# Kernel optimization log

Measured on AMD Instinct MI355X. Metric: run time of the kernel, lower is better.

Reference implementation:

```python
import jax, jax.numpy as jnp
import numpy as np

NUM_EMBEDDINGS = 1024
EMBEDDING_DIM = 256


def setup_inputs() -> dict:
    key = jax.random.key(0)
    k1, k2 = jax.random.split(key)
    z = jax.random.normal(k1, (32, EMBEDDING_DIM, 32, 32), dtype=jnp.float32)
    codebook = jax.random.normal(k2, (NUM_EMBEDDINGS, EMBEDDING_DIM), dtype=jnp.float32)
    return {"z": z, "codebook": codebook}


def reference(z, codebook):
    # z: (B, C, H, W) -> (B, H, W, C) -> (B*H*W, C)
    B, C, H, W = z.shape
    z_bhwc = jnp.transpose(z, (0, 2, 3, 1))
    z_flat = z_bhwc.reshape(-1, C)  # (N, C)

    # pairwise squared distances: ||z||^2 + ||e||^2 - 2 z.e^T  -> (N, K)
    distances = (
        jnp.sum(z_flat ** 2, axis=1, keepdims=True)
        + jnp.sum(codebook ** 2, axis=1)
        - 2.0 * jnp.matmul(z_flat, codebook.T)
    )
    argmin_codewords = jnp.argmin(distances, axis=1)  # (N,)
    min_codewords = jax.nn.one_hot(argmin_codewords, NUM_EMBEDDINGS, dtype=jnp.float32)  # (N, K)

    # quantized latents via one-hot @ codebook, back to (B, C, H, W)
    z_quantized = jnp.matmul(min_codewords, codebook).reshape(B, H, W, C)
    z_quantized = jnp.transpose(z_quantized, (0, 3, 1, 2))
    return (min_codewords, z_quantized)
```

## Files before the change

kernel.cpp:

```cpp
#include <hip/hip_runtime.h>

#define N_ROWS 32768
#define K_CODES 1024
#define CDIM 256

typedef _Float16 half8 __attribute__((ext_vector_type(8)));
typedef _Float16 half4 __attribute__((ext_vector_type(4)));
typedef float floatx16 __attribute__((ext_vector_type(16)));
typedef unsigned long long ull;

#define WS_ZH   0ull
#define WS_ZL   16777216ull
#define WS_CBH  33554432ull
#define WS_CBL  34078720ull
#define WS_CBN  34603008ull
#define WS_PART 34607104ull
#define WS_IDX  36704256ull
#define WS_NEED 36835328ull

__device__ __forceinline__ void g2lds16(const void* g, void* l) {
    __builtin_amdgcn_global_load_lds(
        (const __attribute__((address_space(1))) void*)g,
        (__attribute__((address_space(3))) void*)l, 16, 0, 0);
}


__global__ __launch_bounds__(64) void cb_prep(const float* __restrict__ cb,
                                              _Float16* __restrict__ cbh,
                                              _Float16* __restrict__ cbl,
                                              float* __restrict__ cbn) {
    int k = blockIdx.x;
    int lane = threadIdx.x;
    float4 v = reinterpret_cast<const float4*>(cb + k * CDIM)[lane];
    float s0 = v.x * 32.f, s1 = v.y * 32.f, s2 = v.z * 32.f, s3 = v.w * 32.f;
    half4 hv, lv;
    hv[0] = (_Float16)s0; lv[0] = (_Float16)(s0 - (float)hv[0]);
    hv[1] = (_Float16)s1; lv[1] = (_Float16)(s1 - (float)hv[1]);
    hv[2] = (_Float16)s2; lv[2] = (_Float16)(s2 - (float)hv[2]);
    hv[3] = (_Float16)s3; lv[3] = (_Float16)(s3 - (float)hv[3]);
    size_t off = (size_t)((lane >> 3) * K_CODES + k) * 32 + ((lane * 4) & 31);
    *reinterpret_cast<half4*>(&cbh[off]) = hv;
    *reinterpret_cast<half4*>(&cbl[off]) = lv;
    float s = s0 * s0 + s1 * s1 + s2 * s2 + s3 * s3;
    #pragma unroll
    for (int off2 = 32; off2 > 0; off2 >>= 1) s += __shfl_down(s, off2);
    if (lane == 0) cbn[k] = s;
}

__global__ __launch_bounds__(256) void z_prep(const float* __restrict__ z,
                                              _Float16* __restrict__ zh,
                                              _Float16* __restrict__ zl) {
    __shared__ float t[64][68];
    int hwt = blockIdx.x & 15;
    int ct  = (blockIdx.x >> 4) & 3;
    int bb  = blockIdx.x >> 6;
    int tid = threadIdx.x;
    #pragma unroll
    for (int p = 0; p < 4; p++) {
        int e = p * 256 + tid;
        int c = e >> 4, h4 = e & 15;
        float4 v = *reinterpret_cast<const float4*>(
            &z[((bb * 256 + ct * 64 + c) << 10) + hwt * 64 + h4 * 4]);
        *reinterpret_cast<float4*>(&t[c][h4 * 4]) = v;
    }
    __syncthreads();
    #pragma unroll
    for (int p = 0; p < 4; p++) {
        int e = p * 256 + tid;
        int hw = e >> 4, c4 = e & 15;
        half4 hv, lv;
        #pragma unroll
        for (int j = 0; j < 4; j++) {
            float s = t[c4 * 4 + j][hw] * 32.f;
            _Float16 h = (_Float16)s;
            hv[j] = h;
            lv[j] = (_Float16)(s - (float)h);
        }
        int n = bb * 1024 + hwt * 64 + hw;
        int cg = ct * 64 + c4 * 4;
        size_t off = (size_t)((cg >> 5) * N_ROWS + n) * 32 + (cg & 31);
        *reinterpret_cast<half4*>(&zh[off]) = hv;
        *reinterpret_cast<half4*>(&zl[off]) = lv;
    }
}

__global__ __launch_bounds__(256, 2) void vq_mfma32(
    const _Float16* __restrict__ zh, const _Float16* __restrict__ zl,
    const _Float16* __restrict__ cbh, const _Float16* __restrict__ cbl,
    const float* __restrict__ cbn, ull* __restrict__ partial) {

    __shared__ _Float16 AhL[8192], AlL[8192];
    __shared__ _Float16 BhL[4096], BlL[4096];
    __shared__ float rvv[256][2];
    __shared__ int   rcc[256][2];

    const int tid = threadIdx.x;
    const int lane = tid & 63, wave = tid >> 6;
    const int wm = wave & 1, wn = wave >> 1;
    const int fm = lane & 31, fq = lane >> 5;
    const int codeTile = blockIdx.x & 7;
    const int rowTile  = blockIdx.x >> 3;
    const int rowBase = rowTile * 256, codeBase = codeTile * 128;

    floatx16 acc[8];
    #pragma unroll
    for (int i = 0; i < 8; i++) acc[i] = (floatx16)0.f;

    for (int kc = 0; kc < CDIM; kc += 32) {
        const int cc = kc >> 5;
        const size_t ab = (size_t)(cc * N_ROWS + rowBase) * 32;
        const size_t bb = (size_t)(cc * K_CODES + codeBase) * 32;
        #pragma unroll
        for (int i = 0; i < 4; i++) {
            int G = i * 256 + tid;
            int q = G >> 8, r = G & 255;
            size_t so = (size_t)r * 32 + q * 8;
            g2lds16(zh + ab + so, &AhL[G * 8]);
            g2lds16(zl + ab + so, &AlL[G * 8]);
        }
        #pragma unroll
        for (int i = 0; i < 2; i++) {
            int G = i * 256 + tid;
            int q = G >> 7, r = G & 127;
            size_t so = (size_t)r * 32 + q * 8;
            g2lds16(cbh + bb + so, &BhL[G * 8]);
            g2lds16(cbl + bb + so, &BlL[G * 8]);
        }
        __syncthreads();
        #pragma unroll
        for (int s = 0; s < 2; s++) {
            int q = s * 2 + fq;
            half8 ah[4], al[4], bh[2], bl[2];
            #pragma unroll
            for (int i = 0; i < 4; i++) {
                int ga = q * 256 + wm * 128 + i * 32 + fm;
                ah[i] = *reinterpret_cast<const half8*>(&AhL[ga * 8]);
                al[i] = *reinterpret_cast<const half8*>(&AlL[ga * 8]);
            }
            #pragma unroll
            for (int j = 0; j < 2; j++) {
                int gb = q * 128 + wn * 64 + j * 32 + fm;
                bh[j] = *reinterpret_cast<const half8*>(&BhL[gb * 8]);
                bl[j] = *reinterpret_cast<const half8*>(&BlL[gb * 8]);
            }
            #pragma unroll
            for (int i = 0; i < 4; i++)
                #pragma unroll
                for (int j = 0; j < 2; j++) {
                    acc[i*2+j] = __builtin_amdgcn_mfma_f32_32x32x16_f16(ah[i], bh[j], acc[i*2+j], 0, 0, 0);
                    acc[i*2+j] = __builtin_amdgcn_mfma_f32_32x32x16_f16(al[i], bh[j], acc[i*2+j], 0, 0, 0);
                    acc[i*2+j] = __builtin_amdgcn_mfma_f32_32x32x16_f16(ah[i], bl[j], acc[i*2+j], 0, 0, 0);
                }
        }
        __syncthreads();
    }

    float cbnv[2];
    #pragma unroll
    for (int j = 0; j < 2; j++) cbnv[j] = cbn[codeBase + wn * 64 + j * 32 + fm];

    #pragma unroll
    for (int i = 0; i < 4; i++)
        #pragma unroll
        for (int r = 0; r < 16; r++) {
            float best = 3.4e38f; int bcode = 0x7fffffff;
            #pragma unroll
            for (int j = 0; j < 2; j++) {
                float d = fmaf(-2.f, acc[i*2+j][r], cbnv[j]);
                int code = codeBase + wn * 64 + j * 32 + fm;
                if (d < best) { best = d; bcode = code; }
            }
            #pragma unroll
            for (int m = 1; m < 32; m <<= 1) {
                float ov = __shfl_xor(best, m, 64);
                int   oc = __shfl_xor(bcode, m, 64);
                if (ov < best || (ov == best && oc < bcode)) { best = ov; bcode = oc; }
            }
            if (fm == 0) {
                int row = wm * 128 + i * 32 + (r & 3) + 8 * (r >> 2) + 4 * fq;
                rvv[row][wn] = best;
                rcc[row][wn] = bcode;
            }
        }
    __syncthreads();
    {
        float v0 = rvv[tid][0]; int c0 = rcc[tid][0];
        float v1 = rvv[tid][1]; int c1 = rcc[tid][1];
        if (v1 < v0 || (v1 == v0 && c1 < c0)) { v0 = v1; c0 = c1; }
        unsigned u = __float_as_uint(v0);
        u = (u & 0x80000000u) ? ~u : (u | 0x80000000u);
        partial[(size_t)(rowBase + tid) * 8 + codeTile] =
            ((ull)u << 32) | (unsigned)c0;
    }
}

__global__ __launch_bounds__(256) void onehot_fin(const ull* __restrict__ partial,
                                                  int* __restrict__ idx,
                                                  float* __restrict__ out) {
    int row = blockIdx.x;
    __shared__ int sid;
    if (threadIdx.x < 64) {
        ull v = (threadIdx.x < 8) ? partial[(size_t)row * 8 + threadIdx.x]
                                  : ~0ull;
        #pragma unroll
        for (int m = 1; m < 8; m <<= 1) {
            ull o = __shfl_xor(v, m, 64);
            if (o < v) v = o;
        }
        if (threadIdx.x == 0) {
            int id = (int)(v & 0xffffffffu);
            sid = id;
            idx[row] = id;
        }
    }
    __syncthreads();
    int id = sid;
    int k4 = threadIdx.x << 2;
    float4 v4;
    v4.x = (k4     == id) ? 1.f : 0.f;
    v4.y = (k4 + 1 == id) ? 1.f : 0.f;
    v4.z = (k4 + 2 == id) ? 1.f : 0.f;
    v4.w = (k4 + 3 == id) ? 1.f : 0.f;
    reinterpret_cast<float4*>(out)[(size_t)row * 256 + threadIdx.x] = v4;
}

__global__ __launch_bounds__(256) void zq_fill(const int* __restrict__ idx,
                                               const float* __restrict__ cb,
                                               float* __restrict__ out) {
    int i  = blockIdx.x * 256 + threadIdx.x;
    int hw = i & 1023;
    int c  = (i >> 10) & 255;
    int b  = i >> 18;
    int n  = (b << 10) | hw;
    out[i] = cb[idx[n] * CDIM + c];
}


__global__ __launch_bounds__(64) void cb_norms(const float* __restrict__ cb,
                                               float* __restrict__ cbn) {
    int k = blockIdx.x;
    int lane = threadIdx.x;
    float4 v = reinterpret_cast<const float4*>(cb + k * CDIM)[lane];
    float s = v.x * v.x + v.y * v.y + v.z * v.z + v.w * v.w;
    #pragma unroll
    for (int off = 32; off > 0; off >>= 1) s += __shfl_down(s, off);
    if (lane == 0) cbn[k] = s;
}

__global__ __launch_bounds__(256) void cb_transpose(const float* __restrict__ cb,
                                                    float* __restrict__ cbt) {
    __shared__ float t[32][33];
    int k0 = (blockIdx.x & 31) * 32;
    int c0 = (blockIdx.x >> 5) * 32;
    int lane = threadIdx.x & 31;
    int row = threadIdx.x >> 5;
    #pragma unroll
    for (int s = 0; s < 4; s++) {
        int r = row + s * 8;
        t[r][lane] = cb[(k0 + r) * CDIM + c0 + lane];
    }
    __syncthreads();
    #pragma unroll
    for (int s = 0; s < 4; s++) {
        int r = row + s * 8;
        cbt[(c0 + r) * K_CODES + k0 + lane] = t[lane][r];
    }
}

__global__ __launch_bounds__(512, 2) void vq_argmin(const float* __restrict__ z,
                                                    const float* __restrict__ cbt,
                                                    const float* __restrict__ cbn,
                                                    int* __restrict__ idx_out) {
    __shared__ float As[64][128];
    __shared__ float Bs[64][256];

    const int tid = threadIdx.x;
    const int tx = tid & 31;
    const int ty = tid >> 5;
    const int rowBase = blockIdx.x * 128;
    const int bb = rowBase >> 10;
    const int hwBase = rowBase & 1023;

    float minv[8];
    int   mini[8];
    #pragma unroll
    for (int i = 0; i < 8; i++) { minv[i] = 3.4e38f; mini[i] = 0; }

    for (int kt = 0; kt < K_CODES; kt += 256) {
        float acc[2][2][4][4];
        #pragma unroll
        for (int a = 0; a < 2; a++)
            #pragma unroll
            for (int b = 0; b < 2; b++)
                #pragma unroll
                for (int i = 0; i < 4; i++)
                    #pragma unroll
                    for (int j = 0; j < 4; j++) acc[a][b][i][j] = 0.f;

        for (int ccb = 0; ccb < CDIM; ccb += 64) {
            #pragma unroll
            for (int l = 0; l < 4; l++) {
                int f = tid + l * 512;
                int r4 = f & 31, c = f >> 5;
                float4 v = *reinterpret_cast<const float4*>(
                    &z[((bb * 256 + ccb + c) << 10) + hwBase + r4 * 4]);
                *reinterpret_cast<float4*>(&As[c][r4 * 4]) = v;
            }
            #pragma unroll
            for (int l = 0; l < 8; l++) {
                int f = tid + l * 512;
                int k4 = f & 63, c = f >> 6;
                float4 v = *reinterpret_cast<const float4*>(
                    &cbt[(ccb + c) * K_CODES + kt + k4 * 4]);
                *reinterpret_cast<float4*>(&Bs[c][k4 * 4]) = v;
            }
            __syncthreads();
            #pragma unroll 4
            for (int c = 0; c < 64; c++) {
                float4 a0 = *reinterpret_cast<const float4*>(&As[c][ty * 4]);
                float4 a1 = *reinterpret_cast<const float4*>(&As[c][64 + ty * 4]);
                float4 b0 = *reinterpret_cast<const float4*>(&Bs[c][tx * 4]);
                float4 b1 = *reinterpret_cast<const float4*>(&Bs[c][128 + tx * 4]);
                float av[2][4] = {{a0.x, a0.y, a0.z, a0.w}, {a1.x, a1.y, a1.z, a1.w}};
                float bw[2][4] = {{b0.x, b0.y, b0.z, b0.w}, {b1.x, b1.y, b1.z, b1.w}};
                #pragma unroll
                for (int ri = 0; ri < 2; ri++)
                    #pragma unroll
                    for (int i = 0; i < 4; i++)
                        #pragma unroll
                        for (int ci = 0; ci < 2; ci++)
                            #pragma unroll
                            for (int j = 0; j < 4; j++)
                                acc[ri][ci][i][j] =
                                    fmaf(av[ri][i], bw[ci][j], acc[ri][ci][i][j]);
            }
            __syncthreads();
        }
        #pragma unroll
        for (int ci = 0; ci < 2; ci++)
            #pragma unroll
            for (int j = 0; j < 4; j++) {
                int code = kt + ci * 128 + tx * 4 + j;
                float nrm = cbn[code];
                #pragma unroll
                for (int ri = 0; ri < 2; ri++)
                    #pragma unroll
                    for (int i = 0; i < 4; i++) {
                        float d = fmaf(-2.f, acc[ri][ci][i][j], nrm);
                        int r = ri * 4 + i;
                        if (d < minv[r]) { minv[r] = d; mini[r] = code; }
                    }
            }
    }

    __syncthreads();
    float (*rv)[32] = reinterpret_cast<float(*)[32]>(&As[0][0]);
    int   (*rix)[32] = reinterpret_cast<int(*)[32]>(&As[32][0]);
    #pragma unroll
    for (int ri = 0; ri < 2; ri++)
        #pragma unroll
        for (int i = 0; i < 4; i++) {
            int row = ri * 64 + ty * 4 + i;
            rv[row][tx] = minv[ri * 4 + i];
            rix[row][tx] = mini[ri * 4 + i];
        }
    __syncthreads();
    if (tid < 128) {
        float bvv = rv[tid][0]; int bii = rix[tid][0];
        #pragma unroll
        for (int t = 1; t < 32; t++) {
            float v = rv[tid][t]; int ii = rix[tid][t];
            if (v < bvv || (v == bvv && ii < bii)) { bvv = v; bii = ii; }
        }
        idx_out[rowBase + tid] = bii;
    }
}

__global__ __launch_bounds__(256) void onehot_fill(const int* __restrict__ idx,
                                                   float* __restrict__ out) {
    int i = blockIdx.x * 256 + threadIdx.x;
    int n  = i >> 8;
    int k4 = (i & 255) << 2;
    int id = idx[n];
    float4 v;
    v.x = (k4     == id) ? 1.f : 0.f;
    v.y = (k4 + 1 == id) ? 1.f : 0.f;
    v.z = (k4 + 2 == id) ? 1.f : 0.f;
    v.w = (k4 + 3 == id) ? 1.f : 0.f;
    reinterpret_cast<float4*>(out)[i] = v;
}

extern "C" void kernel_launch(void* const* d_in, const int* in_sizes, int n_in,
                              void* d_out, int out_size, void* d_ws, size_t ws_size,
                              hipStream_t stream) {
    const float* z  = (const float*)d_in[0];
    const float* cb = (const float*)d_in[1];
    float* out0 = (float*)d_out;
    float* out1 = out0 + (size_t)N_ROWS * K_CODES;

    if (ws_size >= WS_NEED) {
        _Float16* zh  = (_Float16*)((char*)d_ws + WS_ZH);
        _Float16* zl  = (_Float16*)((char*)d_ws + WS_ZL);
        _Float16* cbh = (_Float16*)((char*)d_ws + WS_CBH);
        _Float16* cbl = (_Float16*)((char*)d_ws + WS_CBL);
        float* cbn = (float*)((char*)d_ws + WS_CBN);
        ull* part = (ull*)((char*)d_ws + WS_PART);
        int* idx = (int*)((char*)d_ws + WS_IDX);

        cb_prep<<<K_CODES, 64, 0, stream>>>(cb, cbh, cbl, cbn);
        z_prep<<<2048, 256, 0, stream>>>(z, zh, zl);
        vq_mfma32<<<1024, 256, 0, stream>>>(zh, zl, cbh, cbl, cbn, part);
        onehot_fin<<<N_ROWS, 256, 0, stream>>>(part, idx, out0);
        zq_fill<<<(N_ROWS * CDIM) / 256, 256, 0, stream>>>(idx, cb, out1);
    } else {
        float* cbn = (float*)d_ws;
        int*   idx = (int*)((char*)d_ws + 4096);
        float* cbt = (float*)((char*)d_ws + 4096 + 131072);

        cb_norms<<<K_CODES, 64, 0, stream>>>(cb, cbn);
        cb_transpose<<<256, 256, 0, stream>>>(cb, cbt);
        vq_argmin<<<N_ROWS / 128, 512, 0, stream>>>(z, cbt, cbn, idx);
        onehot_fill<<<(N_ROWS * K_CODES / 4) / 256, 256, 0, stream>>>(idx, out0);
        zq_fill<<<(N_ROWS * CDIM) / 256, 256, 0, stream>>>(idx, cb, out1);
    }
}
```

Before: 330.5 us.

## Relayout fp16 split operands into 8-element chunks, remap block order, raise occupancy

Changes the global layout of the hi/lo fp16 operands so that each 8-element channel chunk is contiguous across rows and codes. The global-to-LDS loads then become fully coalesced 16-byte streams, and z_prep now writes half8 instead of half4. The block index is remapped so consecutive blocks share a code tile and spread across row tiles, which is meant to improve L2 reuse. The reduction scratch is aliased into the A tile LDS so launch bounds can request 3 blocks per SM, at the risk of register spills.

```diff
diff --git a/kernel.cpp b/kernel.cpp
--- a/kernel.cpp
+++ b/kernel.cpp
@@ -38,7 +38,9 @@
     hv[1] = (_Float16)s1; lv[1] = (_Float16)(s1 - (float)hv[1]);
     hv[2] = (_Float16)s2; lv[2] = (_Float16)(s2 - (float)hv[2]);
     hv[3] = (_Float16)s3; lv[3] = (_Float16)(s3 - (float)hv[3]);
-    size_t off = (size_t)((lane >> 3) * K_CODES + k) * 32 + ((lane * 4) & 31);
+    int cc = lane >> 3;
+    int q  = (lane >> 1) & 3;
+    size_t off = (size_t)((cc * 4 + q) * K_CODES + k) * 8 + (lane & 1) * 4;
     *reinterpret_cast<half4*>(&cbh[off]) = hv;
     *reinterpret_cast<half4*>(&cbl[off]) = lv;
     float s = s0 * s0 + s1 * s1 + s2 * s2 + s3 * s3;
@@ -64,42 +66,42 @@
         *reinterpret_cast<float4*>(&t[c][h4 * 4]) = v;
     }
     __syncthreads();
-    #pragma unroll
-    for (int p = 0; p < 4; p++) {
-        int e = p * 256 + tid;
-        int hw = e >> 4, c4 = e & 15;
-        half4 hv, lv;
-        #pragma unroll
-        for (int j = 0; j < 4; j++) {
-            float s = t[c4 * 4 + j][hw] * 32.f;
+    int hw = tid & 63, g8 = tid >> 6;
+    int n = bb * 1024 + hwt * 64 + hw;
+    #pragma unroll
+    for (int p = 0; p < 2; p++) {
+        int o = g8 * 2 + p;
+        int cg = ct * 64 + o * 8;
+        int cc = cg >> 5, q = (cg >> 3) & 3;
+        half8 hv, lv;
+        #pragma unroll
+        for (int j = 0; j < 8; j++) {
+            float s = t[o * 8 + j][hw] * 32.f;
             _Float16 h = (_Float16)s;
             hv[j] = h;
             lv[j] = (_Float16)(s - (float)h);
         }
-        int n = bb * 1024 + hwt * 64 + hw;
-        int cg = ct * 64 + c4 * 4;
-        size_t off = (size_t)((cg >> 5) * N_ROWS + n) * 32 + (cg & 31);
-        *reinterpret_cast<half4*>(&zh[off]) = hv;
-        *reinterpret_cast<half4*>(&zl[off]) = lv;
-    }
-}
-
-__global__ __launch_bounds__(256, 2) void vq_mfma32(
+        size_t off = (size_t)((cc * 4 + q) * N_ROWS + n) * 8;
+        *reinterpret_cast<half8*>(&zh[off]) = hv;
+        *reinterpret_cast<half8*>(&zl[off]) = lv;
+    }
+}
+
+__global__ __launch_bounds__(256, 3) void vq_mfma32(
     const _Float16* __restrict__ zh, const _Float16* __restrict__ zl,
     const _Float16* __restrict__ cbh, const _Float16* __restrict__ cbl,
     const float* __restrict__ cbn, ull* __restrict__ partial) {
 
     __shared__ _Float16 AhL[8192], AlL[8192];
     __shared__ _Float16 BhL[4096], BlL[4096];
-    __shared__ float rvv[256][2];
-    __shared__ int   rcc[256][2];
 
     const int tid = threadIdx.x;
     const int lane = tid & 63, wave = tid >> 6;
     const int wm = wave & 1, wn = wave >> 1;
     const int fm = lane & 31, fq = lane >> 5;
-    const int codeTile = blockIdx.x & 7;
-    const int rowTile  = blockIdx.x >> 3;
+    const int codeTile = blockIdx.x >> 7;
+    const int g = blockIdx.x & 127;
+    const int rowTile = (g & 7) * 16 + (g >> 3);
     const int rowBase = rowTile * 256, codeBase = codeTile * 128;
 
     floatx16 acc[8];
@@ -108,23 +110,21 @@
 
     for (int kc = 0; kc < CDIM; kc += 32) {
         const int cc = kc >> 5;
-        const size_t ab = (size_t)(cc * N_ROWS + rowBase) * 32;
-        const size_t bb = (size_t)(cc * K_CODES + codeBase) * 32;
         #pragma unroll
         for (int i = 0; i < 4; i++) {
             int G = i * 256 + tid;
             int q = G >> 8, r = G & 255;
-            size_t so = (size_t)r * 32 + q * 8;
-            g2lds16(zh + ab + so, &AhL[G * 8]);
-            g2lds16(zl + ab + so, &AlL[G * 8]);
+            size_t so = (size_t)((cc * 4 + q) * N_ROWS + rowBase + r) * 8;
+            g2lds16(zh + so, &AhL[G * 8]);
+            g2lds16(zl + so, &AlL[G * 8]);
         }
         #pragma unroll
         for (int i = 0; i < 2; i++) {
             int G = i * 256 + tid;
-            int q = G >> 7, r = G & 127;
-            size_t so = (size_t)r * 32 + q * 8;
-            g2lds16(cbh + bb + so, &BhL[G * 8]);
-            g2lds16(cbl + bb + so, &BlL[G * 8]);
+            int q = G >> 7, c2 = G & 127;
+            size_t so = (size_t)((cc * 4 + q) * K_CODES + codeBase + c2) * 8;
+            g2lds16(cbh + so, &BhL[G * 8]);
+            g2lds16(cbl + so, &BlL[G * 8]);
         }
         __syncthreads();
         #pragma unroll
@@ -154,6 +154,9 @@
         }
         __syncthreads();
     }
+
+    float (*rvv)[2] = reinterpret_cast<float(*)[2]>(&AhL[0]);
+    int   (*rcc)[2] = reinterpret_cast<int(*)[2]>(&AhL[1024]);
 
     float cbnv[2];
     #pragma unroll
```

Result: slower. 354.1 us (+7.1%).
